# Kernel optimization log

Hardware: AMD Instinct MI355X
Metric: run time of the kernel (lower is better)

The kernel has to match this reference:

```python
import math
import jax, jax.numpy as jnp
import numpy as np

B, L, D, H = 2, 1024, 1024, 16
HD = D // H
NBUCKETS = 64
EPS = 1e-5


def _rotary(x, pos):
    # x: (B,H,L,hd), pos: (B,L) float positions
    hd = x.shape[-1]
    nf = hd // 2
    periods = jnp.exp(jnp.linspace(math.log(1.0), math.log(10000.0), nf))
    freqs = 2.0 * np.pi / periods
    freqs = jnp.concatenate([freqs, freqs], axis=-1)  # (hd,)
    ang = pos[:, None, :, None].astype(x.dtype) * freqs  # (B,1,L,hd)
    cos, sin = jnp.cos(ang), jnp.sin(ang)
    x1, x2 = jnp.split(x, 2, axis=-1)
    rot = jnp.concatenate([-x2, x1], axis=-1)
    return x * cos + rot * sin


def _layernorm(x, g, b):
    mu = jnp.mean(x, axis=-1, keepdims=True)
    var = jnp.mean((x - mu) ** 2, axis=-1, keepdims=True)
    return (x - mu) * jax.lax.rsqrt(var + EPS) * g + b


def setup_inputs() -> dict:
    key = jax.random.key(0)
    ks = jax.random.split(key, 16)
    s = 1.0 / math.sqrt(D)
    x = jax.random.normal(ks[0], (B, L, D), jnp.float32)
    z = jax.random.randint(ks[1], (B, L, L), 0, NBUCKETS, jnp.int32)
    mask = jnp.ones((B, L), dtype=bool)
    idx = jnp.tile(jnp.arange(L, dtype=jnp.int32)[None, :], (B, 1))
    chain = jnp.sort(jax.random.randint(ks[2], (B, L), 0, 4, jnp.int32), axis=-1)
    mol_type = jax.random.randint(ks[3], (B, L), 0, 2, jnp.int32)
    Wq = jax.random.normal(ks[4], (D, D), jnp.float32) * s
    Wk = jax.random.normal(ks[5], (D, D), jnp.float32) * s
    Wv = jax.random.normal(ks[6], (D, D), jnp.float32) * s
    Wo = jax.random.normal(ks[7], (D, D), jnp.float32) * s
    cWq = jax.random.normal(ks[8], (D, D), jnp.float32) * s
    cWk = jax.random.normal(ks[9], (D, D), jnp.float32) * s
    cWv = jax.random.normal(ks[10], (D, D), jnp.float32) * s
    qg = jnp.ones((D,), jnp.float32)
    qb = jnp.zeros((D,), jnp.float32)
    kg = jnp.ones((D,), jnp.float32)
    kb = jnp.zeros((D,), jnp.float32)
    attn_bias = jax.random.normal(ks[11], (NBUCKETS, H), jnp.float32) * 0.02
    return dict(x=x, z=z, mask=mask, idx=idx, chain=chain, mol_type=mol_type,
                Wq=Wq, Wk=Wk, Wv=Wv, Wo=Wo, cWq=cWq, cWk=cWk, cWv=cWv,
                qg=qg, qb=qb, kg=kg, kb=kb, attn_bias=attn_bias)


def reference(x, z, mask, idx, chain, mol_type, Wq, Wk, Wv, Wo, cWq, cWk, cWv,
              qg, qb, kg, kb, attn_bias):
    scale = 1.0 / math.sqrt(HD)  # sqrt(D / heads)

    def split_heads(t):  # (B,L,D) -> (B,H,L,hd)
        return t.reshape(B, L, H, HD).transpose(0, 2, 1, 3)

    q = split_heads(_layernorm(x @ Wq.T, qg, qb))
    k = split_heads(_layernorm(x @ Wk.T, kg, kb))
    q = _rotary(q, idx)
    k = _rotary(k, idx)
    attn = jnp.einsum('bhqd,bhkd->bhqk', q, k) * scale

    cq = split_heads(x @ cWq.T)
    ck = split_heads(x @ cWk.T)
    cross_attn = jnp.einsum('bhqd,bhkd->bhqk', cq, ck) * scale

    # same polymer chain mask (B,L,L)
    spm = (chain[:, None, :] == chain[:, :, None]) & (mol_type == 0)[:, None, :]
    attn = jnp.where(spm[:, None], attn, cross_attn)

    # gathered pairwise bias: bias[z] (B,L,L,H) -> (B,H,L,L)
    attn = attn + attn_bias[z].transpose(0, 3, 1, 2)

    attn = jnp.where(mask[:, None, None, :], attn, -jnp.inf)
    attn = jax.nn.softmax(attn, axis=-1)

    self_w = jnp.where(spm[:, None], attn, 0.0)
    cross_w = jnp.where(spm[:, None], 0.0, attn)

    v = split_heads(x @ Wv.T)
    v = _rotary(v, idx)  # rope_values
    out = jnp.einsum('bhqk,bhkd->bhqd', self_w, v)
    out = _rotary(out, -idx)
    out = out.transpose(0, 2, 1, 3).reshape(B, L, D)

    cv = split_heads(x @ cWv.T)
    cross_out = jnp.einsum('bhqk,bhkd->bhqd', cross_w, cv)
    cross_out = cross_out.transpose(0, 2, 1, 3).reshape(B, L, D)

    return (out + cross_out) @ Wo.T
```

## Files before the change

kernel.cpp:

```cpp
#include <hip/hip_runtime.h>


typedef __attribute__((ext_vector_type(8))) short short8;
typedef __attribute__((ext_vector_type(4))) short short4v;
typedef __attribute__((ext_vector_type(4))) float f32x4;

struct W6 { const unsigned short* p[6]; };
struct Src13 { const void* p[13]; };

__device__ __forceinline__ float bf2f(unsigned short u){
  union { unsigned u32; float f; } v; v.u32 = ((unsigned)u) << 16; return v.f;
}
__device__ __forceinline__ unsigned short f2bf(float f){
  unsigned u = __float_as_uint(f);
  u += 0x7FFFu + ((u >> 16) & 1u);
  return (unsigned short)(u >> 16);
}
__device__ __forceinline__ unsigned short f2bf_rz(float f){
  return (unsigned short)(__float_as_uint(f) >> 16);
}
__device__ __forceinline__ void async16(const void* g, void* l){
  __builtin_amdgcn_global_load_lds(
      (const __attribute__((address_space(1))) unsigned int*)g,
      (__attribute__((address_space(3))) unsigned int*)l, 16, 0, 0);
}
__device__ __forceinline__ f32x4 mfma16(short8 a, short8 b, f32x4 c){
  return __builtin_amdgcn_mfma_f32_16x16x32_bf16(a, b, c, 0, 0, 0);
}
__device__ __forceinline__ float freq_of(int dd){
  return 6.283185307179586f * __expf(-0.29710775393471563f * (float)dd);
}

#define PX   0
#define PW(i) (2097152 + (i) * 1048576)
#define PQG  9437184
#define PQB  9438208
#define PKG  9439232
#define PKB  9440256
#define PBI  9441280
#define PARK_TOTAL 9442304

__global__ __launch_bounds__(256) void k_convert(
    Src13 src, unsigned short* __restrict__ park,
    const int* __restrict__ z, unsigned char* __restrict__ zpk,
    int* __restrict__ flag)
{
  const int t = threadIdx.x;
  const int bid = blockIdx.x;
  if (bid >= 9221) {
    int base = (bid - 9221) * 1024 + t * 4;
    int4 zv = *(const int4*)(z + base);
    unsigned int pk = (unsigned)zv.x | ((unsigned)zv.y << 8) |
                      ((unsigned)zv.z << 16) | ((unsigned)zv.w << 24);
    *(unsigned int*)(zpk + base) = pk;
    return;
  }
  __shared__ int shcnt;
  if (t == 0) shcnt = 0;
  __syncthreads();
  const unsigned short* xr = (const unsigned short*)src.p[0];
  int e = (xr[2 * t] >> 7) & 0xFF;
  unsigned long long m = __ballot(e >= 132);
  if ((t & 63) == 0) atomicAdd(&shcnt, __popcll(m));
  __syncthreads();
  const bool isf32 = shcnt > 64;

  int seg, inner;
  if (bid < 2048)      { seg = 0;                        inner = bid; }
  else if (bid < 9216) { seg = 1 + ((bid - 2048) >> 10); inner = (bid - 2048) & 1023; }
  else                 { seg = 8 + (bid - 9216);         inner = 0; }
  static const __device__ int segbase[13] = {
    PX, PW(0), PW(1), PW(2), PW(3), PW(4), PW(5), PW(6),
    PQG, PQB, PKG, PKB, PBI };
  unsigned short* dst = park + segbase[seg] + inner * 1024 + t * 4;
  if (isf32) {
    const float* s = (const float*)src.p[seg] + inner * 1024 + t * 4;
    f32x4 v = *(const f32x4*)s;
    short4v o;
    o.x = (short)f2bf(v.x); o.y = (short)f2bf(v.y);
    o.z = (short)f2bf(v.z); o.w = (short)f2bf(v.w);
    *(short4v*)dst = o;
  } else {
    const unsigned short* s = (const unsigned short*)src.p[seg] + inner * 1024 + t * 4;
    *(short4v*)dst = *(const short4v*)s;
  }
  if (bid == 0 && t == 0) *flag = isf32 ? 1 : 0;
}

__global__ __launch_bounds__(256, 2) void k_proj_gemm(
    const unsigned short* __restrict__ X, W6 w6, unsigned short* __restrict__ Y)
{
  __shared__ unsigned short As[128 * 32];
  __shared__ unsigned short Bs[128 * 32];
  const int t = threadIdx.x;
  const int lane = t & 63, wid = t >> 6;
  const int m0 = blockIdx.x * 128;
  const int bn = blockIdx.y;
  const unsigned short* W = w6.p[bn >> 3];
  const int nw0 = (bn & 7) * 128;
  const int waveM = (wid & 1) * 64, waveN = (wid >> 1) * 64;
  const int g = lane >> 4, c16 = lane & 15;
  const int srow = t >> 2, scol = (t & 3) * 8;

  f32x4 acc[4][4];
  #pragma unroll
  for (int i = 0; i < 4; i++)
    #pragma unroll
    for (int j = 0; j < 4; j++) acc[i][j] = f32x4{0.f, 0.f, 0.f, 0.f};

  for (int k0 = 0; k0 < 1024; k0 += 32) {
    async16(X + (size_t)(m0 + srow) * 1024 + k0 + scol,       (char*)As + t * 16);
    async16(X + (size_t)(m0 + 64 + srow) * 1024 + k0 + scol,  (char*)As + 4096 + t * 16);
    async16(W + (size_t)(nw0 + srow) * 1024 + k0 + scol,      (char*)Bs + t * 16);
    async16(W + (size_t)(nw0 + 64 + srow) * 1024 + k0 + scol, (char*)Bs + 4096 + t * 16);
    __syncthreads();
    short8 af[4], bfr[4];
    #pragma unroll
    for (int mt = 0; mt < 4; mt++)
      af[mt] = *(const short8*)(As + (waveM + mt * 16 + c16) * 32 + g * 8);
    #pragma unroll
    for (int nt = 0; nt < 4; nt++)
      bfr[nt] = *(const short8*)(Bs + (waveN + nt * 16 + c16) * 32 + g * 8);
    #pragma unroll
    for (int mt = 0; mt < 4; mt++)
      #pragma unroll
      for (int nt = 0; nt < 4; nt++)
        acc[mt][nt] = mfma16(af[mt], bfr[nt], acc[mt][nt]);
    __syncthreads();
  }
  const int n0 = bn * 128;
  #pragma unroll
  for (int mt = 0; mt < 4; mt++)
    #pragma unroll
    for (int nt = 0; nt < 4; nt++)
      #pragma unroll
      for (int r = 0; r < 4; r++) {
        int row = m0 + waveM + mt * 16 + g * 4 + r;
        int col = n0 + waveN + nt * 16 + c16;
        Y[(size_t)row * 6144 + col] = f2bf(acc[mt][nt][r]);
      }
}

__global__ __launch_bounds__(256) void k_post(
    const unsigned short* __restrict__ Y,
    const unsigned short* __restrict__ qg, const unsigned short* __restrict__ qbv,
    const unsigned short* __restrict__ kg, const unsigned short* __restrict__ kbv,
    const int* __restrict__ idx,
    unsigned short* __restrict__ qo, unsigned short* __restrict__ ko,
    unsigned short* __restrict__ cqo, unsigned short* __restrict__ cko,
    unsigned short* __restrict__ vto, unsigned short* __restrict__ cvto)
{
  const int r = blockIdx.x;
  const int b = r >> 10, l = r & 1023;
  const int t = threadIdx.x;
  __shared__ float red[4];
  __shared__ float rowbuf[1024];
  __shared__ float tc[32], ts[32];
  const unsigned short* Yr = Y + (size_t)r * 6144;
  const float pos = (float)idx[r];

  if (t < 32) {
    float a = pos * freq_of(t);
    tc[t] = cosf(a);
    ts[t] = sinf(a);
  }
  __syncthreads();

  for (int sec = 0; sec < 2; sec++) {
    const unsigned short* src = Yr + sec * 1024;
    const unsigned short* gg = sec ? kg : qg;
    const unsigned short* bb = sec ? kbv : qbv;
    unsigned short* dst = sec ? ko : qo;
    float v0 = bf2f(src[t]), v1 = bf2f(src[t + 256]);
    float v2 = bf2f(src[t + 512]), v3 = bf2f(src[t + 768]);
    float s = v0 + v1 + v2 + v3;
    float s2 = v0 * v0 + v1 * v1 + v2 * v2 + v3 * v3;
    #pragma unroll
    for (int o = 32; o > 0; o >>= 1) {
      s += __shfl_down(s, o, 64);
      s2 += __shfl_down(s2, o, 64);
    }
    __syncthreads();
    if ((t & 63) == 0) red[t >> 6] = s;
    __syncthreads();
    float tot = red[0] + red[1] + red[2] + red[3];
    __syncthreads();
    if ((t & 63) == 0) red[t >> 6] = s2;
    __syncthreads();
    float tot2 = red[0] + red[1] + red[2] + red[3];
    float mu = tot * (1.f / 1024.f);
    float var = tot2 * (1.f / 1024.f) - mu * mu;
    float rstd = rsqrtf(var + 1e-5f);
    rowbuf[t]       = (v0 - mu) * rstd * bf2f(gg[t])       + bf2f(bb[t]);
    rowbuf[t + 256] = (v1 - mu) * rstd * bf2f(gg[t + 256]) + bf2f(bb[t + 256]);
    rowbuf[t + 512] = (v2 - mu) * rstd * bf2f(gg[t + 512]) + bf2f(bb[t + 512]);
    rowbuf[t + 768] = (v3 - mu) * rstd * bf2f(gg[t + 768]) + bf2f(bb[t + 768]);
    __syncthreads();
    #pragma unroll
    for (int j = 0; j < 4; j++) {
      int d = t + 256 * j;
      int h = d >> 6, dd = d & 63;
      float c = tc[dd & 31], sn = ts[dd & 31];
      float x1 = rowbuf[d];
      float x2 = rowbuf[(d & ~63) | ((dd + 32) & 63)];
      float res = (dd < 32) ? (x1 * c - x2 * sn) : (x1 * c + x2 * sn);
      dst[((size_t)(b * 16 + h) * 1024 + l) * 64 + dd] = f2bf(res);
    }
  }
  {
    const unsigned short* src = Yr + 2048;
    __syncthreads();
    rowbuf[t] = bf2f(src[t]); rowbuf[t + 256] = bf2f(src[t + 256]);
    rowbuf[t + 512] = bf2f(src[t + 512]); rowbuf[t + 768] = bf2f(src[t + 768]);
    __syncthreads();
    #pragma unroll
    for (int j = 0; j < 4; j++) {
      int d = t + 256 * j;
      int h = d >> 6, dd = d & 63;
      float c = tc[dd & 31], sn = ts[dd & 31];
      float x1 = rowbuf[d];
      float x2 = rowbuf[(d & ~63) | ((dd + 32) & 63)];
      float res = (dd < 32) ? (x1 * c - x2 * sn) : (x1 * c + x2 * sn);
      vto[((size_t)(b * 16 + h) * 64 + dd) * 1024 + l] = f2bf(res);
    }
  }
  #pragma unroll
  for (int j = 0; j < 4; j++) {
    int d = t + 256 * j;
    int h = d >> 6, dd = d & 63;
    size_t km = ((size_t)(b * 16 + h) * 1024 + l) * 64 + dd;
    cqo[km] = Yr[3072 + d];
    cko[km] = Yr[4096 + d];
    cvto[((size_t)(b * 16 + h) * 64 + dd) * 1024 + l] = Yr[5120 + d];
  }
}

__global__ __launch_bounds__(256, 2) void k_attn(
    const unsigned short* __restrict__ qm, const unsigned short* __restrict__ km,
    const unsigned short* __restrict__ cqm, const unsigned short* __restrict__ ckm,
    const unsigned short* __restrict__ vt, const unsigned short* __restrict__ cvt,
    const int* __restrict__ chain, const int* __restrict__ mol,
    const unsigned char* __restrict__ zpk, const unsigned short* __restrict__ bias,
    float* __restrict__ Opart, float* __restrict__ lpart)
{
  const int q0 = blockIdx.x * 128;
  const int bh = blockIdx.y;
  const int seg = blockIdx.z;
  const int b = bh >> 4, h = bh & 15;
  __shared__ float biasf[64];
  __shared__ unsigned char codek[512];
  __shared__ __align__(16) unsigned char zs[128 * 64];
  __shared__ __align__(16) unsigned short Ks[64 * 64], cKs[64 * 64];
  __shared__ __align__(16) unsigned short Vs[64 * 64], cVs[64 * 64];
  __shared__ unsigned short Ps[4][16][36];
  __shared__ unsigned short Pc[4][16][36];
  const int t = threadIdx.x, lane = t & 63, w = t >> 6;
  const int g = lane >> 4, c16 = lane & 15;
  const int kbeg = seg * 512;

  if (t < 128) {
    int4 ch = *(const int4*)(chain + b * 1024 + kbeg + t * 4);
    int4 mo = *(const int4*)(mol   + b * 1024 + kbeg + t * 4);
    codek[t * 4 + 0] = mo.x ? 255 : (unsigned char)ch.x;
    codek[t * 4 + 1] = mo.y ? 255 : (unsigned char)ch.y;
    codek[t * 4 + 2] = mo.z ? 255 : (unsigned char)ch.z;
    codek[t * 4 + 3] = mo.w ? 255 : (unsigned char)ch.w;
  } else if (t < 192) {
    biasf[t - 128] = bf2f(bias[(t - 128) * 16 + h]);
  }

  const size_t basep = (size_t)bh << 16;
  int cqa[2][4];
  #pragma unroll
  for (int s = 0; s < 2; s++) {
    int4 cqv = *(const int4*)(chain + b * 1024 + q0 + s * 64 + w * 16 + g * 4);
    cqa[s][0] = cqv.x; cqa[s][1] = cqv.y; cqa[s][2] = cqv.z; cqa[s][3] = cqv.w;
  }

  float l_[2][4];
  f32x4 Os[2][4], Oc[2][4];
  #pragma unroll
  for (int s = 0; s < 2; s++)
    #pragma unroll
    for (int nt = 0; nt < 4; nt++) {
      l_[s][nt] = 0.f;
      Os[s][nt] = f32x4{0.f, 0.f, 0.f, 0.f};
      Oc[s][nt] = f32x4{0.f, 0.f, 0.f, 0.f};
    }
  const int Rk = t >> 3, jk = t & 7;
  const int Rz = t >> 2, jz = t & 3;
  const f32x4 zero = f32x4{0.f, 0.f, 0.f, 0.f};
  __syncthreads();

  for (int kc = 0; kc < 8; kc++) {
    const int kt = kbeg + kc * 64;
    #pragma unroll
    for (int i = 0; i < 2; i++)
      async16(zpk + (size_t)b * 1048576 + (size_t)(q0 + i * 64 + Rz) * 1024
                  + kt + jz * 16,
              (char*)zs + i * 4096 + t * 16);
    #pragma unroll
    for (int i = 0; i < 2; i++) {
      int row = i * 32 + Rk;
      int srcb = jk ^ (row & 7);
      async16(km  + basep + (size_t)(kt + row) * 64 + srcb * 8, (char*)Ks  + i * 4096 + t * 16);
      async16(ckm + basep + (size_t)(kt + row) * 64 + srcb * 8, (char*)cKs + i * 4096 + t * 16);
      async16(vt  + basep + (size_t)row * 1024 + kt + srcb * 8, (char*)Vs  + i * 4096 + t * 16);
      async16(cvt + basep + (size_t)row * 1024 + kt + srcb * 8, (char*)cVs + i * 4096 + t * 16);
    }
    __syncthreads();
    #pragma unroll
    for (int s = 0; s < 2; s++) {
      const int rb = q0 + s * 64 + w * 16;
      const unsigned short* qrow  = qm  + basep + (size_t)(rb + c16) * 64;
      const unsigned short* cqrow = cqm + basep + (size_t)(rb + c16) * 64;
      short8 aq0  = *(const short8*)(qrow + g * 8);
      short8 aq1  = *(const short8*)(qrow + 32 + g * 8);
      short8 acq0 = *(const short8*)(cqrow + g * 8);
      short8 acq1 = *(const short8*)(cqrow + 32 + g * 8);
      f32x4 sS[4], sC[4];
      #pragma unroll
      for (int n = 0; n < 4; n++) {
        int R = n * 16 + c16;
        int sw = R & 7;
        short8 kbl = *(const short8*)((char*)Ks  + R * 128 + ((g ^ sw) * 16));
        short8 kbh = *(const short8*)((char*)Ks  + R * 128 + (((4 + g) ^ sw) * 16));
        short8 cbl = *(const short8*)((char*)cKs + R * 128 + ((g ^ sw) * 16));
        short8 cbh = *(const short8*)((char*)cKs + R * 128 + (((4 + g) ^ sw) * 16));
        sS[n] = mfma16(aq1, kbh, mfma16(aq0, kbl, zero));
        sC[n] = mfma16(acq1, cbh, mfma16(acq0, cbl, zero));
      }
      #pragma unroll
      for (int half = 0; half < 2; half++) {
        int cd0 = codek[kc * 64 + half * 32 + c16];
        int cd1 = codek[kc * 64 + half * 32 + 16 + c16];
        #pragma unroll
        for (int r = 0; r < 4; r++) {
          const unsigned char* zr = zs + (s * 64 + w * 16 + g * 4 + r) * 64 + half * 32;
          float bi0 = biasf[zr[c16]];
          float bi1 = biasf[zr[16 + c16]];
          bool sp0 = (cd0 == cqa[s][r]);
          bool sp1 = (cd1 == cqa[s][r]);
          int n0 = half * 2, n1 = half * 2 + 1;
          float p0 = __expf(__fmaf_rn(sp0 ? sS[n0][r] : sC[n0][r], 0.125f, bi0));
          float p1 = __expf(__fmaf_rn(sp1 ? sS[n1][r] : sC[n1][r], 0.125f, bi1));
          l_[s][r] += p0 + p1;
          int lr = g * 4 + r;
          Ps[w][lr][c16]      = f2bf_rz(sp0 ? p0 : 0.f);
          Pc[w][lr][c16]      = f2bf_rz(sp0 ? 0.f : p0);
          Ps[w][lr][16 + c16] = f2bf_rz(sp1 ? p1 : 0.f);
          Pc[w][lr][16 + c16] = f2bf_rz(sp1 ? 0.f : p1);
        }
        short8 aps = *(const short8*)&Ps[w][c16][g * 8];
        short8 apc = *(const short8*)&Pc[w][c16][g * 8];
        #pragma unroll
        for (int nt = 0; nt < 4; nt++) {
          int R = nt * 16 + c16;
          int sw = R & 7;
          int J = half * 4 + g;
          short8 bv  = *(const short8*)((char*)Vs  + R * 128 + ((J ^ sw) * 16));
          short8 bcv = *(const short8*)((char*)cVs + R * 128 + ((J ^ sw) * 16));
          Os[s][nt] = mfma16(aps, bv,  Os[s][nt]);
          Oc[s][nt] = mfma16(apc, bcv, Oc[s][nt]);
        }
      }
    }
    __syncthreads();
  }
  #pragma unroll
  for (int s = 0; s < 2; s++)
    #pragma unroll
    for (int r = 0; r < 4; r++) {
      float lv = l_[s][r];
      lv += __shfl_xor(lv, 1);
      lv += __shfl_xor(lv, 2);
      lv += __shfl_xor(lv, 4);
      lv += __shfl_xor(lv, 8);
      int row = q0 + s * 64 + w * 16 + g * 4 + r;
      float* op = Opart + (((size_t)seg * 32 + bh) * 1024 + row) * 128;
      #pragma unroll
      for (int nt = 0; nt < 4; nt++) {
        op[nt * 16 + c16]      = Os[s][nt][r];
        op[64 + nt * 16 + c16] = Oc[s][nt][r];
      }
      if (c16 == 0) lpart[((size_t)seg * 32 + bh) * 1024 + row] = lv;
    }
}

__global__ __launch_bounds__(256) void k_combine(
    const float* __restrict__ Opart, const float* __restrict__ lpart,
    const int* __restrict__ idx, unsigned short* __restrict__ comb)
{
  const int t = threadIdx.x;
  const int rg = blockIdx.x * 8 + (t >> 5);
  const int d = t & 31;
  const int bh = rg >> 10, row = rg & 1023;
  const int b = bh >> 4, h = bh & 15;
  float oslo = 0.f, oshi = 0.f, oclo = 0.f, ochi = 0.f, l = 0.f;
  #pragma unroll
  for (int seg = 0; seg < 2; seg++) {
    const float* op = Opart + (((size_t)seg * 32 + bh) * 1024 + row) * 128;
    oslo += op[d]; oshi += op[32 + d];
    oclo += op[64 + d]; ochi += op[96 + d];
    l += lpart[((size_t)seg * 32 + bh) * 1024 + row];
  }
  float inv = 1.f / l;
  float pos = (float)idx[b * 1024 + row];
  float fr = freq_of(d);
  float aa = -pos * fr;
  float cc = cosf(aa), sn = sinf(aa);
  size_t orow = ((size_t)(b * 1024 + row)) * 1024 + h * 64;
  comb[orow + d]      = f2bf((oslo * cc - oshi * sn + oclo) * inv);
  comb[orow + d + 32] = f2bf((oshi * cc + oslo * sn + ochi) * inv);
}

__global__ __launch_bounds__(256, 2) void k_out_gemm(
    const unsigned short* __restrict__ A, const unsigned short* __restrict__ Wo,
    const int* __restrict__ flag, void* __restrict__ outv)
{
  __shared__ unsigned short As[128 * 32];
  __shared__ unsigned short Bs[128 * 32];
  const int t = threadIdx.x;
  const int lane = t & 63, wid = t >> 6;
  const int m0 = blockIdx.x * 128;
  const int n0 = blockIdx.y * 128;
  const int waveM = (wid & 1) * 64, waveN = (wid >> 1) * 64;
  const int g = lane >> 4, c16 = lane & 15;
  const int srow = t >> 2, scol = (t & 3) * 8;
  const int f32out = *flag;
  f32x4 acc[4][4];
  #pragma unroll
  for (int i = 0; i < 4; i++)
    #pragma unroll
    for (int j = 0; j < 4; j++) acc[i][j] = f32x4{0.f, 0.f, 0.f, 0.f};
  for (int k0 = 0; k0 < 1024; k0 += 32) {
    async16(A  + (size_t)(m0 + srow) * 1024 + k0 + scol,       (char*)As + t * 16);
    async16(A  + (size_t)(m0 + 64 + srow) * 1024 + k0 + scol,  (char*)As + 4096 + t * 16);
    async16(Wo + (size_t)(n0 + srow) * 1024 + k0 + scol,       (char*)Bs + t * 16);
    async16(Wo + (size_t)(n0 + 64 + srow) * 1024 + k0 + scol,  (char*)Bs + 4096 + t * 16);
    __syncthreads();
    short8 af[4], bfr[4];
    #pragma unroll
    for (int mt = 0; mt < 4; mt++)
      af[mt] = *(const short8*)(As + (waveM + mt * 16 + c16) * 32 + g * 8);
    #pragma unroll
    for (int nt = 0; nt < 4; nt++)
      bfr[nt] = *(const short8*)(Bs + (waveN + nt * 16 + c16) * 32 + g * 8);
    #pragma unroll
    for (int mt = 0; mt < 4; mt++)
      #pragma unroll
      for (int nt = 0; nt < 4; nt++)
        acc[mt][nt] = mfma16(af[mt], bfr[nt], acc[mt][nt]);
    __syncthreads();
  }
  #pragma unroll
  for (int mt = 0; mt < 4; mt++)
    #pragma unroll
    for (int nt = 0; nt < 4; nt++)
      #pragma unroll
      for (int r = 0; r < 4; r++) {
        int row = m0 + waveM + mt * 16 + g * 4 + r;
        int col = n0 + waveN + nt * 16 + c16;
        if (f32out) ((float*)outv)[(size_t)row * 1024 + col] = acc[mt][nt][r];
        else ((unsigned short*)outv)[(size_t)row * 1024 + col] = f2bf(acc[mt][nt][r]);
      }
}

extern "C" void kernel_launch(void* const* d_in, const int* in_sizes, int n_in,
                              void* d_out, int out_size, void* d_ws, size_t ws_size,
                              hipStream_t stream)
{
  (void)in_sizes; (void)n_in; (void)out_size; (void)ws_size;
  const int* z     = (const int*)d_in[1];
  const int* idx   = (const int*)d_in[3];
  const int* chain = (const int*)d_in[4];
  const int* mol   = (const int*)d_in[5];

  char* ws = (char*)d_ws;
  unsigned short* Y     = (unsigned short*)ws;
  size_t off = 50331648;
  unsigned short* qbuf  = (unsigned short*)(ws + off); off += 4194304;
  unsigned short* kbuf  = (unsigned short*)(ws + off); off += 4194304;
  unsigned short* cqbuf = (unsigned short*)(ws + off); off += 4194304;
  unsigned short* ckbuf = (unsigned short*)(ws + off); off += 4194304;
  unsigned short* vtbuf = (unsigned short*)(ws + off); off += 4194304;
  unsigned short* cvtbuf= (unsigned short*)(ws + off); off += 4194304;
  unsigned short* comb  = (unsigned short*)(ws + off); off += 4194304;
  unsigned short* park  = (unsigned short*)(ws + off); off += (size_t)PARK_TOTAL * 2;
  unsigned char*  zpk   = (unsigned char*)(ws + off); off += 2097152;
  float*          Opart = (float*)(ws + off); off += (size_t)2 * 32 * 1024 * 128 * 4;
  float*          lpart = (float*)(ws + off); off += (size_t)2 * 32 * 1024 * 4;
  int*            flag  = (int*)(ws + off);

  Src13 src;
  src.p[0]  = d_in[0];
  src.p[1]  = d_in[6];
  src.p[2]  = d_in[7];
  src.p[3]  = d_in[8];
  src.p[4]  = d_in[9];
  src.p[5]  = d_in[10];
  src.p[6]  = d_in[11];
  src.p[7]  = d_in[12];
  src.p[8]  = d_in[13];
  src.p[9]  = d_in[14];
  src.p[10] = d_in[15];
  src.p[11] = d_in[16];
  src.p[12] = d_in[17];

  W6 w6;
  w6.p[0] = park + PW(0);
  w6.p[1] = park + PW(1);
  w6.p[2] = park + PW(2);
  w6.p[3] = park + PW(4);
  w6.p[4] = park + PW(5);
  w6.p[5] = park + PW(6);

  k_convert<<<11269, 256, 0, stream>>>(src, park, z, zpk, flag);
  k_proj_gemm<<<dim3(16, 48), 256, 0, stream>>>(park + PX, w6, Y);
  k_post<<<2048, 256, 0, stream>>>(Y, park + PQG, park + PQB, park + PKG, park + PKB,
                                   idx, qbuf, kbuf, cqbuf, ckbuf, vtbuf, cvtbuf);
  k_attn<<<dim3(8, 32, 2), 256, 0, stream>>>(qbuf, kbuf, cqbuf, ckbuf, vtbuf, cvtbuf,
                                             chain, mol, zpk, park + PBI,
                                             Opart, lpart);
  k_combine<<<4096, 256, 0, stream>>>(Opart, lpart, idx, comb);
  k_out_gemm<<<dim3(16, 8), 256, 0, stream>>>(comb, park + PW(3), flag, d_out);
}
```

Baseline: 250.1 us.

## Double-buffer attention K/V/z tiles and enlarge blocks to 512 threads

The attention kernel now runs 512 threads per block covering 256 query rows, and double-buffers the K, cK, V, cV and z-code tiles in LDS. The next chunk is prefetched asynchronously while the current one is computed, with waits handled by explicit vmcnt and barriers. Q fragments are loaded once into registers instead of on every key chunk, and the z tile gets an XOR swizzle to reduce LDS bank conflicts. The cost is roughly double the LDS footprint and half as many blocks, which may lower occupancy and parallelism across the GPU.

```diff
diff --git a/kernel.cpp b/kernel.cpp
--- a/kernel.cpp
+++ b/kernel.cpp
@@ -235,7 +235,7 @@
   }
 }
 
-__global__ __launch_bounds__(256, 2) void k_attn(
+__global__ __launch_bounds__(512, 2) void k_attn(
     const unsigned short* __restrict__ qm, const unsigned short* __restrict__ km,
     const unsigned short* __restrict__ cqm, const unsigned short* __restrict__ ckm,
     const unsigned short* __restrict__ vt, const unsigned short* __restrict__ cvt,
@@ -243,17 +243,17 @@
     const unsigned char* __restrict__ zpk, const unsigned short* __restrict__ bias,
     float* __restrict__ Opart, float* __restrict__ lpart)
 {
-  const int q0 = blockIdx.x * 128;
+  const int q0 = blockIdx.x * 256;
   const int bh = blockIdx.y;
   const int seg = blockIdx.z;
   const int b = bh >> 4, h = bh & 15;
   __shared__ float biasf[64];
   __shared__ unsigned char codek[512];
-  __shared__ __align__(16) unsigned char zs[128 * 64];
-  __shared__ __align__(16) unsigned short Ks[64 * 64], cKs[64 * 64];
-  __shared__ __align__(16) unsigned short Vs[64 * 64], cVs[64 * 64];
-  __shared__ unsigned short Ps[4][16][36];
-  __shared__ unsigned short Pc[4][16][36];
+  __shared__ __align__(16) unsigned char zs[2][256 * 64];
+  __shared__ __align__(16) unsigned short Ks[2][64 * 64], cKs[2][64 * 64];
+  __shared__ __align__(16) unsigned short Vs[2][64 * 64], cVs[2][64 * 64];
+  __shared__ unsigned short Ps[8][16][36];
+  __shared__ unsigned short Pc[8][16][36];
   const int t = threadIdx.x, lane = t & 63, w = t >> 6;
   const int g = lane >> 4, c16 = lane & 15;
   const int kbeg = seg * 512;
@@ -273,8 +273,19 @@
   int cqa[2][4];
   #pragma unroll
   for (int s = 0; s < 2; s++) {
-    int4 cqv = *(const int4*)(chain + b * 1024 + q0 + s * 64 + w * 16 + g * 4);
+    int4 cqv = *(const int4*)(chain + b * 1024 + q0 + s * 128 + w * 16 + g * 4);
     cqa[s][0] = cqv.x; cqa[s][1] = cqv.y; cqa[s][2] = cqv.z; cqa[s][3] = cqv.w;
+  }
+
+  short8 aq0[2], aq1[2], acq0[2], acq1[2];
+  #pragma unroll
+  for (int s = 0; s < 2; s++) {
+    const unsigned short* qrow  = qm  + basep + (size_t)(q0 + s * 128 + w * 16 + c16) * 64;
+    const unsigned short* cqrow = cqm + basep + (size_t)(q0 + s * 128 + w * 16 + c16) * 64;
+    aq0[s]  = *(const short8*)(qrow + g * 8);
+    aq1[s]  = *(const short8*)(qrow + 32 + g * 8);
+    acq0[s] = *(const short8*)(cqrow + g * 8);
+    acq1[s] = *(const short8*)(cqrow + 32 + g * 8);
   }
 
   float l_[2][4];
@@ -289,46 +300,50 @@
     }
   const int Rk = t >> 3, jk = t & 7;
   const int Rz = t >> 2, jz = t & 3;
+  const int swk8  = (jk ^ (Rk & 7)) * 8;
+  const int swz16 = (jz ^ ((Rz >> 2) & 3)) * 16;
   const f32x4 zero = f32x4{0.f, 0.f, 0.f, 0.f};
+
+#define STAGE(bi, kcn) do { \
+    const int kt_ = kbeg + (kcn) * 64; \
+    async16(zpk + (size_t)b * 1048576 + (size_t)(q0 + Rz) * 1024 + kt_ + swz16, \
+            (char*)zs[bi] + t * 16); \
+    async16(zpk + (size_t)b * 1048576 + (size_t)(q0 + 128 + Rz) * 1024 + kt_ + swz16, \
+            (char*)zs[bi] + 8192 + t * 16); \
+    async16(km  + basep + (size_t)(kt_ + Rk) * 64 + swk8, (char*)Ks[bi]  + t * 16); \
+    async16(ckm + basep + (size_t)(kt_ + Rk) * 64 + swk8, (char*)cKs[bi] + t * 16); \
+    async16(vt  + basep + (size_t)Rk * 1024 + kt_ + swk8, (char*)Vs[bi]  + t * 16); \
+    async16(cvt + basep + (size_t)Rk * 1024 + kt_ + swk8, (char*)cVs[bi] + t * 16); \
+  } while (0)
+
+  STAGE(0, 0);
   __syncthreads();
 
   for (int kc = 0; kc < 8; kc++) {
-    const int kt = kbeg + kc * 64;
-    #pragma unroll
-    for (int i = 0; i < 2; i++)
-      async16(zpk + (size_t)b * 1048576 + (size_t)(q0 + i * 64 + Rz) * 1024
-                  + kt + jz * 16,
-              (char*)zs + i * 4096 + t * 16);
-    #pragma unroll
-    for (int i = 0; i < 2; i++) {
-      int row = i * 32 + Rk;
-      int srcb = jk ^ (row & 7);
-      async16(km  + basep + (size_t)(kt + row) * 64 + srcb * 8, (char*)Ks  + i * 4096 + t * 16);
-      async16(ckm + basep + (size_t)(kt + row) * 64 + srcb * 8, (char*)cKs + i * 4096 + t * 16);
-      async16(vt  + basep + (size_t)row * 1024 + kt + srcb * 8, (char*)Vs  + i * 4096 + t * 16);
-      async16(cvt + basep + (size_t)row * 1024 + kt + srcb * 8, (char*)cVs + i * 4096 + t * 16);
-    }
-    __syncthreads();
+    const int cur = kc & 1;
+    if (kc < 7) {
+      STAGE(cur ^ 1, kc + 1);
+      __builtin_amdgcn_sched_barrier(0);
+      asm volatile("s_waitcnt vmcnt(6)" ::: "memory");
+    } else {
+      __builtin_amdgcn_sched_barrier(0);
+      asm volatile("s_waitcnt vmcnt(0)" ::: "memory");
+    }
+    __builtin_amdgcn_s_barrier();
+    __builtin_amdgcn_sched_barrier(0);
     #pragma unroll
     for (int s = 0; s < 2; s++) {
-      const int rb = q0 + s * 64 + w * 16;
-      const unsigned short* qrow  = qm  + basep + (size_t)(rb + c16) * 64;
-      const unsigned short* cqrow = cqm + basep + (size_t)(rb + c16) * 64;
-      short8 aq0  = *(const short8*)(qrow + g * 8);
-      short8 aq1  = *(const short8*)(qrow + 32 + g * 8);
-      short8 acq0 = *(const short8*)(cqrow + g * 8);
-      short8 acq1 = *(const short8*)(cqrow + 32 + g * 8);
       f32x4 sS[4], sC[4];
       #pragma unroll
       for (int n = 0; n < 4; n++) {
         int R = n * 16 + c16;
         int sw = R & 7;
-        short8 kbl = *(const short8*)((char*)Ks  + R * 128 + ((g ^ sw) * 16));
-        short8 kbh = *(const short8*)((char*)Ks  + R * 128 + (((4 + g) ^ sw) * 16));
-        short8 cbl = *(const short8*)((char*)cKs + R * 128 + ((g ^ sw) * 16));
-        short8 cbh = *(const short8*)((char*)cKs + R * 128 + (((4 + g) ^ sw) * 16));
-        sS[n] = mfma16(aq1, kbh, mfma16(aq0, kbl, zero));
-        sC[n] = mfma16(acq1, cbh, mfma16(acq0, cbl, zero));
+        short8 kbl = *(const short8*)((char*)Ks[cur]  + R * 128 + ((g ^ sw) * 16));
+        short8 kbh = *(const short8*)((char*)Ks[cur]  + R * 128 + (((4 + g) ^ sw) * 16));
+        short8 cbl = *(const short8*)((char*)cKs[cur] + R * 128 + ((g ^ sw) * 16));
+        short8 cbh = *(const short8*)((char*)cKs[cur] + R * 128 + (((4 + g) ^ sw) * 16));
+        sS[n] = mfma16(aq1[s], kbh, mfma16(aq0[s], kbl, zero));
+        sC[n] = mfma16(acq1[s], cbh, mfma16(acq0[s], cbl, zero));
       }
       #pragma unroll
       for (int half = 0; half < 2; half++) {
@@ -336,9 +351,9 @@
         int cd1 = codek[kc * 64 + half * 32 + 16 + c16];
         #pragma unroll
         for (int r = 0; r < 4; r++) {
-          const unsigned char* zr = zs + (s * 64 + w * 16 + g * 4 + r) * 64 + half * 32;
-          float bi0 = biasf[zr[c16]];
-          float bi1 = biasf[zr[16 + c16]];
+          const unsigned char* zr = zs[cur] + (s * 128 + w * 16 + g * 4 + r) * 64;
+          float bi0 = biasf[zr[((half * 2) ^ g) * 16 + c16]];
+          float bi1 = biasf[zr[((half * 2 + 1) ^ g) * 16 + c16]];
           bool sp0 = (cd0 == cqa[s][r]);
           bool sp1 = (cd1 == cqa[s][r]);
           int n0 = half * 2, n1 = half * 2 + 1;
@@ -358,15 +373,18 @@
           int R = nt * 16 + c16;
           int sw = R & 7;
           int J = half * 4 + g;
-          short8 bv  = *(const short8*)((char*)Vs  + R * 128 + ((J ^ sw) * 16));
-          short8 bcv = *(const short8*)((char*)cVs + R * 128 + ((J ^ sw) * 16));
+          short8 bv  = *(const short8*)((char*)Vs[cur]  + R * 128 + ((J ^ sw) * 16));
+          short8 bcv = *(const short8*)((char*)cVs[cur] + R * 128 + ((J ^ sw) * 16));
           Os[s][nt] = mfma16(aps, bv,  Os[s][nt]);
           Oc[s][nt] = mfma16(apc, bcv, Oc[s][nt]);
         }
       }
     }
-    __syncthreads();
-  }
+    __builtin_amdgcn_sched_barrier(0);
+    __builtin_amdgcn_s_barrier();
+  }
+#undef STAGE
+
   #pragma unroll
   for (int s = 0; s < 2; s++)
     #pragma unroll
@@ -376,7 +394,7 @@
       lv += __shfl_xor(lv, 2);
       lv += __shfl_xor(lv, 4);
       lv += __shfl_xor(lv, 8);
-      int row = q0 + s * 64 + w * 16 + g * 4 + r;
+      int row = q0 + s * 128 + w * 16 + g * 4 + r;
       float* op = Opart + (((size_t)seg * 32 + bh) * 1024 + row) * 128;
       #pragma unroll
       for (int nt = 0; nt < 4; nt++) {
@@ -519,7 +537,7 @@
   k_proj_gemm<<<dim3(16, 48), 256, 0, stream>>>(park + PX, w6, Y);
   k_post<<<2048, 256, 0, stream>>>(Y, park + PQG, park + PQB, park + PKG, park + PKB,
                                    idx, qbuf, kbuf, cqbuf, ckbuf, vtbuf, cvtbuf);
-  k_attn<<<dim3(8, 32, 2), 256, 0, stream>>>(qbuf, kbuf, cqbuf, ckbuf, vtbuf, cvtbuf,
+  k_attn<<<dim3(4, 32, 2), 512, 0, stream>>>(qbuf, kbuf, cqbuf, ckbuf, vtbuf, cvtbuf,
                                              chain, mol, zpk, park + PBI,
                                              Opart, lpart);
   k_combine<<<4096, 256, 0, stream>>>(Opart, lpart, idx, comb);
```

New measurement: 249.6 us. Within noise of the previous version (-0.2%).

## Halve attention query tile to 64 rows, hoist Q fragments, swizzle z tile

Applied to the files above, without the earlier changes.

The attention kernel now processes 64 query rows per block instead of 128, which doubles the grid to 1024 blocks and raises the launch-bounds occupancy hint from 2 to 3 blocks per CU. Q and cQ fragments are loaded once into registers before the key loop instead of being reloaded from global memory on every chunk. The z-bucket tile in LDS is XOR-swizzled to reduce bank conflicts on the bias lookup. The trade-off is that each K/V tile is now loaded by twice as many blocks, so K/V traffic increases while per-block register and LDS footprint shrink.

```diff
diff --git a/kernel.cpp b/kernel.cpp
--- a/kernel.cpp
+++ b/kernel.cpp
@@ -235,7 +235,7 @@
   }
 }
 
-__global__ __launch_bounds__(256, 2) void k_attn(
+__global__ __launch_bounds__(256, 3) void k_attn(
     const unsigned short* __restrict__ qm, const unsigned short* __restrict__ km,
     const unsigned short* __restrict__ cqm, const unsigned short* __restrict__ ckm,
     const unsigned short* __restrict__ vt, const unsigned short* __restrict__ cvt,
@@ -243,17 +243,16 @@
     const unsigned char* __restrict__ zpk, const unsigned short* __restrict__ bias,
     float* __restrict__ Opart, float* __restrict__ lpart)
 {
-  const int q0 = blockIdx.x * 128;
+  const int q0 = blockIdx.x * 64;
   const int bh = blockIdx.y;
   const int seg = blockIdx.z;
   const int b = bh >> 4, h = bh & 15;
   __shared__ float biasf[64];
   __shared__ unsigned char codek[512];
-  __shared__ __align__(16) unsigned char zs[128 * 64];
+  __shared__ __align__(16) unsigned char zs[64 * 64];
   __shared__ __align__(16) unsigned short Ks[64 * 64], cKs[64 * 64];
   __shared__ __align__(16) unsigned short Vs[64 * 64], cVs[64 * 64];
-  __shared__ unsigned short Ps[4][16][36];
-  __shared__ unsigned short Pc[4][16][36];
+  __shared__ unsigned short Ps[4][16][36], Pc[4][16][36];
   const int t = threadIdx.x, lane = t & 63, w = t >> 6;
   const int g = lane >> 4, c16 = lane & 15;
   const int kbeg = seg * 512;
@@ -270,35 +269,37 @@
   }
 
   const size_t basep = (size_t)bh << 16;
-  int cqa[2][4];
-  #pragma unroll
-  for (int s = 0; s < 2; s++) {
-    int4 cqv = *(const int4*)(chain + b * 1024 + q0 + s * 64 + w * 16 + g * 4);
-    cqa[s][0] = cqv.x; cqa[s][1] = cqv.y; cqa[s][2] = cqv.z; cqa[s][3] = cqv.w;
-  }
-
-  float l_[2][4];
-  f32x4 Os[2][4], Oc[2][4];
-  #pragma unroll
-  for (int s = 0; s < 2; s++)
-    #pragma unroll
-    for (int nt = 0; nt < 4; nt++) {
-      l_[s][nt] = 0.f;
-      Os[s][nt] = f32x4{0.f, 0.f, 0.f, 0.f};
-      Oc[s][nt] = f32x4{0.f, 0.f, 0.f, 0.f};
-    }
+  int cqa[4];
+  {
+    int4 cqv = *(const int4*)(chain + b * 1024 + q0 + w * 16 + g * 4);
+    cqa[0] = cqv.x; cqa[1] = cqv.y; cqa[2] = cqv.z; cqa[3] = cqv.w;
+  }
+
+  const unsigned short* qrow  = qm  + basep + (size_t)(q0 + w * 16 + c16) * 64;
+  const unsigned short* cqrow = cqm + basep + (size_t)(q0 + w * 16 + c16) * 64;
+  short8 aq0  = *(const short8*)(qrow + g * 8);
+  short8 aq1  = *(const short8*)(qrow + 32 + g * 8);
+  short8 acq0 = *(const short8*)(cqrow + g * 8);
+  short8 acq1 = *(const short8*)(cqrow + 32 + g * 8);
+
+  float l_[4];
+  f32x4 Os[4], Oc[4];
+  #pragma unroll
+  for (int nt = 0; nt < 4; nt++) {
+    l_[nt] = 0.f;
+    Os[nt] = f32x4{0.f, 0.f, 0.f, 0.f};
+    Oc[nt] = f32x4{0.f, 0.f, 0.f, 0.f};
+  }
   const int Rk = t >> 3, jk = t & 7;
   const int Rz = t >> 2, jz = t & 3;
+  const int swz16 = (jz ^ ((Rz >> 2) & 3)) * 16;
   const f32x4 zero = f32x4{0.f, 0.f, 0.f, 0.f};
   __syncthreads();
 
   for (int kc = 0; kc < 8; kc++) {
     const int kt = kbeg + kc * 64;
-    #pragma unroll
-    for (int i = 0; i < 2; i++)
-      async16(zpk + (size_t)b * 1048576 + (size_t)(q0 + i * 64 + Rz) * 1024
-                  + kt + jz * 16,
-              (char*)zs + i * 4096 + t * 16);
+    async16(zpk + (size_t)b * 1048576 + (size_t)(q0 + Rz) * 1024 + kt + swz16,
+            (char*)zs + t * 16);
     #pragma unroll
     for (int i = 0; i < 2; i++) {
       int row = i * 32 + Rk;
@@ -309,82 +310,71 @@
       async16(cvt + basep + (size_t)row * 1024 + kt + srcb * 8, (char*)cVs + i * 4096 + t * 16);
     }
     __syncthreads();
-    #pragma unroll
-    for (int s = 0; s < 2; s++) {
-      const int rb = q0 + s * 64 + w * 16;
-      const unsigned short* qrow  = qm  + basep + (size_t)(rb + c16) * 64;
-      const unsigned short* cqrow = cqm + basep + (size_t)(rb + c16) * 64;
-      short8 aq0  = *(const short8*)(qrow + g * 8);
-      short8 aq1  = *(const short8*)(qrow + 32 + g * 8);
-      short8 acq0 = *(const short8*)(cqrow + g * 8);
-      short8 acq1 = *(const short8*)(cqrow + 32 + g * 8);
-      f32x4 sS[4], sC[4];
+    f32x4 sS[4], sC[4];
+    #pragma unroll
+    for (int n = 0; n < 4; n++) {
+      int R = n * 16 + c16;
+      int sw = R & 7;
+      short8 kbl = *(const short8*)((char*)Ks  + R * 128 + ((g ^ sw) * 16));
+      short8 kbh = *(const short8*)((char*)Ks  + R * 128 + (((4 + g) ^ sw) * 16));
+      short8 cbl = *(const short8*)((char*)cKs + R * 128 + ((g ^ sw) * 16));
+      short8 cbh = *(const short8*)((char*)cKs + R * 128 + (((4 + g) ^ sw) * 16));
+      sS[n] = mfma16(aq1, kbh, mfma16(aq0, kbl, zero));
+      sC[n] = mfma16(acq1, cbh, mfma16(acq0, cbl, zero));
+    }
+    #pragma unroll
+    for (int half = 0; half < 2; half++) {
+      int cd0 = codek[kc * 64 + half * 32 + c16];
+      int cd1 = codek[kc * 64 + half * 32 + 16 + c16];
       #pragma unroll
-      for (int n = 0; n < 4; n++) {
-        int R = n * 16 + c16;
-        int sw = R & 7;
-        short8 kbl = *(const short8*)((char*)Ks  + R * 128 + ((g ^ sw) * 16));
-        short8 kbh = *(const short8*)((char*)Ks  + R * 128 + (((4 + g) ^ sw) * 16));
-        short8 cbl = *(const short8*)((char*)cKs + R * 128 + ((g ^ sw) * 16));
-        short8 cbh = *(const short8*)((char*)cKs + R * 128 + (((4 + g) ^ sw) * 16));
-        sS[n] = mfma16(aq1, kbh, mfma16(aq0, kbl, zero));
-        sC[n] = mfma16(acq1, cbh, mfma16(acq0, cbl, zero));
+      for (int r = 0; r < 4; r++) {
+        const unsigned char* zr = zs + (w * 16 + g * 4 + r) * 64;
+        float bi0 = biasf[zr[((half * 2) ^ g) * 16 + c16]];
+        float bi1 = biasf[zr[((half * 2 + 1) ^ g) * 16 + c16]];
+        bool sp0 = (cd0 == cqa[r]);
+        bool sp1 = (cd1 == cqa[r]);
+        int n0 = half * 2, n1 = half * 2 + 1;
+        float p0 = __expf(__fmaf_rn(sp0 ? sS[n0][r] : sC[n0][r], 0.125f, bi0));
+        float p1 = __expf(__fmaf_rn(sp1 ? sS[n1][r] : sC[n1][r], 0.125f, bi1));
+        l_[r] += p0 + p1;
+        int lr = g * 4 + r;
+        Ps[w][lr][c16]      = f2bf_rz(sp0 ? p0 : 0.f);
+        Pc[w][lr][c16]      = f2bf_rz(sp0 ? 0.f : p0);
+        Ps[w][lr][16 + c16] = f2bf_rz(sp1 ? p1 : 0.f);
+        Pc[w][lr][16 + c16] = f2bf_rz(sp1 ? 0.f : p1);
       }
-      #pragma unroll
-      for (int half = 0; half < 2; half++) {
-        int cd0 = codek[kc * 64 + half * 32 + c16];
-        int cd1 = codek[kc * 64 + half * 32 + 16 + c16];
-        #pragma unroll
-        for (int r = 0; r < 4; r++) {
-          const unsigned char* zr = zs + (s * 64 + w * 16 + g * 4 + r) * 64 + half * 32;
-          float bi0 = biasf[zr[c16]];
-          float bi1 = biasf[zr[16 + c16]];
-          bool sp0 = (cd0 == cqa[s][r]);
-          bool sp1 = (cd1 == cqa[s][r]);
-          int n0 = half * 2, n1 = half * 2 + 1;
-          float p0 = __expf(__fmaf_rn(sp0 ? sS[n0][r] : sC[n0][r], 0.125f, bi0));
-          float p1 = __expf(__fmaf_rn(sp1 ? sS[n1][r] : sC[n1][r], 0.125f, bi1));
-          l_[s][r] += p0 + p1;
-          int lr = g * 4 + r;
-          Ps[w][lr][c16]      = f2bf_rz(sp0 ? p0 : 0.f);
-          Pc[w][lr][c16]      = f2bf_rz(sp0 ? 0.f : p0);
-          Ps[w][lr][16 + c16] = f2bf_rz(sp1 ? p1 : 0.f);
-          Pc[w][lr][16 + c16] = f2bf_rz(sp1 ? 0.f : p1);
-        }
-        short8 aps = *(const short8*)&Ps[w][c16][g * 8];
-        short8 apc = *(const short8*)&Pc[w][c16][g * 8];
-        #pragma unroll
-        for (int nt = 0; nt < 4; nt++) {
-          int R = nt * 16 + c16;
-          int sw = R & 7;
-          int J = half * 4 + g;
-          short8 bv  = *(const short8*)((char*)Vs  + R * 128 + ((J ^ sw) * 16));
-          short8 bcv = *(const short8*)((char*)cVs + R * 128 + ((J ^ sw) * 16));
-          Os[s][nt] = mfma16(aps, bv,  Os[s][nt]);
-          Oc[s][nt] = mfma16(apc, bcv, Oc[s][nt]);
-        }
-      }
-    }
-    __syncthreads();
-  }
-  #pragma unroll
-  for (int s = 0; s < 2; s++)
-    #pragma unroll
-    for (int r = 0; r < 4; r++) {
-      float lv = l_[s][r];
-      lv += __shfl_xor(lv, 1);
-      lv += __shfl_xor(lv, 2);
-      lv += __shfl_xor(lv, 4);
-      lv += __shfl_xor(lv, 8);
-      int row = q0 + s * 64 + w * 16 + g * 4 + r;
-      float* op = Opart + (((size_t)seg * 32 + bh) * 1024 + row) * 128;
+      short8 aps = *(const short8*)&Ps[w][c16][g * 8];
+      short8 apc = *(const short8*)&Pc[w][c16][g * 8];
       #pragma unroll
       for (int nt = 0; nt < 4; nt++) {
-        op[nt * 16 + c16]      = Os[s][nt][r];
-        op[64 + nt * 16 + c16] = Oc[s][nt][r];
+        int R = nt * 16 + c16;
+        int sw = R & 7;
+        int J = half * 4 + g;
+        short8 bv  = *(const short8*)((char*)Vs  + R * 128 + ((J ^ sw) * 16));
+        short8 bcv = *(const short8*)((char*)cVs + R * 128 + ((J ^ sw) * 16));
+        Os[nt] = mfma16(aps, bv,  Os[nt]);
+        Oc[nt] = mfma16(apc, bcv, Oc[nt]);
       }
-      if (c16 == 0) lpart[((size_t)seg * 32 + bh) * 1024 + row] = lv;
-    }
+    }
+    __syncthreads();
+  }
+
+  #pragma unroll
+  for (int r = 0; r < 4; r++) {
+    float lv = l_[r];
+    lv += __shfl_xor(lv, 1);
+    lv += __shfl_xor(lv, 2);
+    lv += __shfl_xor(lv, 4);
+    lv += __shfl_xor(lv, 8);
+    int row = q0 + w * 16 + g * 4 + r;
+    float* op = Opart + (((size_t)seg * 32 + bh) * 1024 + row) * 128;
+    #pragma unroll
+    for (int nt = 0; nt < 4; nt++) {
+      op[nt * 16 + c16]      = Os[nt][r];
+      op[64 + nt * 16 + c16] = Oc[nt][r];
+    }
+    if (c16 == 0) lpart[((size_t)seg * 32 + bh) * 1024 + row] = lv;
+  }
 }
 
 __global__ __launch_bounds__(256) void k_combine(
@@ -519,9 +509,9 @@
   k_proj_gemm<<<dim3(16, 48), 256, 0, stream>>>(park + PX, w6, Y);
   k_post<<<2048, 256, 0, stream>>>(Y, park + PQG, park + PQB, park + PKG, park + PKB,
                                    idx, qbuf, kbuf, cqbuf, ckbuf, vtbuf, cvtbuf);
-  k_attn<<<dim3(8, 32, 2), 256, 0, stream>>>(qbuf, kbuf, cqbuf, ckbuf, vtbuf, cvtbuf,
-                                             chain, mol, zpk, park + PBI,
-                                             Opart, lpart);
+  k_attn<<<dim3(16, 32, 2), 256, 0, stream>>>(qbuf, kbuf, cqbuf, ckbuf, vtbuf, cvtbuf,
+                                              chain, mol, zpk, park + PBI,
+                                              Opart, lpart);
   k_combine<<<4096, 256, 0, stream>>>(Opart, lpart, idx, comb);
   k_out_gemm<<<dim3(16, 8), 256, 0, stream>>>(comb, park + PW(3), flag, d_out);
 }
```

Result: slower. 256.4 us (+2.5%).

## Hoist Q fragments to registers, share K/V LDS loads across sub-tiles, swizzle z tile

Applied to the files above, without the earlier changes.

Q and cross-Q fragments are now loaded from global memory once before the key loop instead of on every key chunk. The loop is reordered so each K and V fragment read from LDS feeds the MFMAs of both 64-row query sub-tiles, halving LDS reads for K/V. P buffers get a per-subtile dimension. The z bucket tile is stored XOR-swizzled in LDS to reduce bank conflicts on the bias gather. The cost is higher register pressure, which may hurt occupancy under the 256x2 launch bounds.

```diff
diff --git a/kernel.cpp b/kernel.cpp
--- a/kernel.cpp
+++ b/kernel.cpp
@@ -252,8 +252,7 @@
   __shared__ __align__(16) unsigned char zs[128 * 64];
   __shared__ __align__(16) unsigned short Ks[64 * 64], cKs[64 * 64];
   __shared__ __align__(16) unsigned short Vs[64 * 64], cVs[64 * 64];
-  __shared__ unsigned short Ps[4][16][36];
-  __shared__ unsigned short Pc[4][16][36];
+  __shared__ unsigned short Ps[4][2][16][36], Pc[4][2][16][36];
   const int t = threadIdx.x, lane = t & 63, w = t >> 6;
   const int g = lane >> 4, c16 = lane & 15;
   const int kbeg = seg * 512;
@@ -277,6 +276,17 @@
     cqa[s][0] = cqv.x; cqa[s][1] = cqv.y; cqa[s][2] = cqv.z; cqa[s][3] = cqv.w;
   }
 
+  short8 aq0[2], aq1[2], acq0[2], acq1[2];
+  #pragma unroll
+  for (int s = 0; s < 2; s++) {
+    const unsigned short* qrow  = qm  + basep + (size_t)(q0 + s * 64 + w * 16 + c16) * 64;
+    const unsigned short* cqrow = cqm + basep + (size_t)(q0 + s * 64 + w * 16 + c16) * 64;
+    aq0[s]  = *(const short8*)(qrow + g * 8);
+    aq1[s]  = *(const short8*)(qrow + 32 + g * 8);
+    acq0[s] = *(const short8*)(cqrow + g * 8);
+    acq1[s] = *(const short8*)(cqrow + 32 + g * 8);
+  }
+
   float l_[2][4];
   f32x4 Os[2][4], Oc[2][4];
   #pragma unroll
@@ -289,6 +299,7 @@
     }
   const int Rk = t >> 3, jk = t & 7;
   const int Rz = t >> 2, jz = t & 3;
+  const int swz16 = (jz ^ ((Rz >> 2) & 3)) * 16;
   const f32x4 zero = f32x4{0.f, 0.f, 0.f, 0.f};
   __syncthreads();
 
@@ -297,7 +308,7 @@
     #pragma unroll
     for (int i = 0; i < 2; i++)
       async16(zpk + (size_t)b * 1048576 + (size_t)(q0 + i * 64 + Rz) * 1024
-                  + kt + jz * 16,
+                  + kt + swz16,
               (char*)zs + i * 4096 + t * 16);
     #pragma unroll
     for (int i = 0; i < 2; i++) {
@@ -310,63 +321,63 @@
     }
     __syncthreads();
     #pragma unroll
-    for (int s = 0; s < 2; s++) {
-      const int rb = q0 + s * 64 + w * 16;
-      const unsigned short* qrow  = qm  + basep + (size_t)(rb + c16) * 64;
-      const unsigned short* cqrow = cqm + basep + (size_t)(rb + c16) * 64;
-      short8 aq0  = *(const short8*)(qrow + g * 8);
-      short8 aq1  = *(const short8*)(qrow + 32 + g * 8);
-      short8 acq0 = *(const short8*)(cqrow + g * 8);
-      short8 acq1 = *(const short8*)(cqrow + 32 + g * 8);
-      f32x4 sS[4], sC[4];
-      #pragma unroll
-      for (int n = 0; n < 4; n++) {
-        int R = n * 16 + c16;
+    for (int half = 0; half < 2; half++) {
+      f32x4 sS[2][2], sC[2][2];
+      #pragma unroll
+      for (int nn = 0; nn < 2; nn++) {
+        int R = (half * 2 + nn) * 16 + c16;
         int sw = R & 7;
         short8 kbl = *(const short8*)((char*)Ks  + R * 128 + ((g ^ sw) * 16));
         short8 kbh = *(const short8*)((char*)Ks  + R * 128 + (((4 + g) ^ sw) * 16));
         short8 cbl = *(const short8*)((char*)cKs + R * 128 + ((g ^ sw) * 16));
         short8 cbh = *(const short8*)((char*)cKs + R * 128 + (((4 + g) ^ sw) * 16));
-        sS[n] = mfma16(aq1, kbh, mfma16(aq0, kbl, zero));
-        sC[n] = mfma16(acq1, cbh, mfma16(acq0, cbl, zero));
+        #pragma unroll
+        for (int s = 0; s < 2; s++) {
+          sS[s][nn] = mfma16(aq1[s], kbh, mfma16(aq0[s], kbl, zero));
+          sC[s][nn] = mfma16(acq1[s], cbh, mfma16(acq0[s], cbl, zero));
+        }
       }
-      #pragma unroll
-      for (int half = 0; half < 2; half++) {
-        int cd0 = codek[kc * 64 + half * 32 + c16];
-        int cd1 = codek[kc * 64 + half * 32 + 16 + c16];
+      int cd0 = codek[kc * 64 + half * 32 + c16];
+      int cd1 = codek[kc * 64 + half * 32 + 16 + c16];
+      short8 aps[2], apc[2];
+      #pragma unroll
+      for (int s = 0; s < 2; s++) {
         #pragma unroll
         for (int r = 0; r < 4; r++) {
-          const unsigned char* zr = zs + (s * 64 + w * 16 + g * 4 + r) * 64 + half * 32;
-          float bi0 = biasf[zr[c16]];
-          float bi1 = biasf[zr[16 + c16]];
+          const unsigned char* zr = zs + (s * 64 + w * 16 + g * 4 + r) * 64;
+          float bi0 = biasf[zr[((half * 2) ^ g) * 16 + c16]];
+          float bi1 = biasf[zr[((half * 2 + 1) ^ g) * 16 + c16]];
           bool sp0 = (cd0 == cqa[s][r]);
           bool sp1 = (cd1 == cqa[s][r]);
-          int n0 = half * 2, n1 = half * 2 + 1;
-          float p0 = __expf(__fmaf_rn(sp0 ? sS[n0][r] : sC[n0][r], 0.125f, bi0));
-          float p1 = __expf(__fmaf_rn(sp1 ? sS[n1][r] : sC[n1][r], 0.125f, bi1));
+          float p0 = __expf(__fmaf_rn(sp0 ? sS[s][0][r] : sC[s][0][r], 0.125f, bi0));
+          float p1 = __expf(__fmaf_rn(sp1 ? sS[s][1][r] : sC[s][1][r], 0.125f, bi1));
           l_[s][r] += p0 + p1;
           int lr = g * 4 + r;
-          Ps[w][lr][c16]      = f2bf_rz(sp0 ? p0 : 0.f);
-          Pc[w][lr][c16]      = f2bf_rz(sp0 ? 0.f : p0);
-          Ps[w][lr][16 + c16] = f2bf_rz(sp1 ? p1 : 0.f);
-          Pc[w][lr][16 + c16] = f2bf_rz(sp1 ? 0.f : p1);
+          Ps[w][s][lr][c16]      = f2bf_rz(sp0 ? p0 : 0.f);
+          Pc[w][s][lr][c16]      = f2bf_rz(sp0 ? 0.f : p0);
+          Ps[w][s][lr][16 + c16] = f2bf_rz(sp1 ? p1 : 0.f);
+          Pc[w][s][lr][16 + c16] = f2bf_rz(sp1 ? 0.f : p1);
         }
-        short8 aps = *(const short8*)&Ps[w][c16][g * 8];
-        short8 apc = *(const short8*)&Pc[w][c16][g * 8];
+        aps[s] = *(const short8*)&Ps[w][s][c16][g * 8];
+        apc[s] = *(const short8*)&Pc[w][s][c16][g * 8];
+      }
+      #pragma unroll
+      for (int nt = 0; nt < 4; nt++) {
+        int R = nt * 16 + c16;
+        int sw = R & 7;
+        int J = half * 4 + g;
+        short8 bv  = *(const short8*)((char*)Vs  + R * 128 + ((J ^ sw) * 16));
+        short8 bcv = *(const short8*)((char*)cVs + R * 128 + ((J ^ sw) * 16));
         #pragma unroll
-        for (int nt = 0; nt < 4; nt++) {
-          int R = nt * 16 + c16;
-          int sw = R & 7;
-          int J = half * 4 + g;
-          short8 bv  = *(const short8*)((char*)Vs  + R * 128 + ((J ^ sw) * 16));
-          short8 bcv = *(const short8*)((char*)cVs + R * 128 + ((J ^ sw) * 16));
-          Os[s][nt] = mfma16(aps, bv,  Os[s][nt]);
-          Oc[s][nt] = mfma16(apc, bcv, Oc[s][nt]);
+        for (int s = 0; s < 2; s++) {
+          Os[s][nt] = mfma16(aps[s], bv,  Os[s][nt]);
+          Oc[s][nt] = mfma16(apc[s], bcv, Oc[s][nt]);
         }
       }
     }
     __syncthreads();
   }
+
   #pragma unroll
   for (int s = 0; s < 2; s++)
     #pragma unroll
```

Result: no change. 252.0 us (+0.8%).
